# Optimization experiments

Hardware: AMD Instinct MI355X
Metric: run time of the kernel (lower is better)

## Reference

```python
import jax, jax.numpy as jnp
import numpy as np

WH, WW = 7, 7
N_WIN_TOKENS = WH * WW
NUM_HEADS = 8
DIM = 256
HEAD_DIM = DIM // NUM_HEADS
SCALE = HEAD_DIM ** -0.5


def _relative_position_index(wh, ww):
    ch = np.arange(wh)
    cw = np.arange(ww)
    coords = np.stack(np.meshgrid(ch, cw, indexing='ij')).reshape(2, -1)  # [2, N]
    rel = coords[:, :, None] - coords[:, None, :]                         # [2, N, N]
    rel = rel.transpose(1, 2, 0).copy()                                   # [N, N, 2]
    rel[..., 0] += wh - 1
    rel[..., 1] += ww - 1
    rel[..., 0] *= 2 * ww - 1
    return jnp.asarray(rel.sum(-1))                                       # [N, N] int

REL_IDX = _relative_position_index(WH, WW)


def setup_inputs() -> dict:
    key = jax.random.key(0)
    ks = jax.random.split(key, 7)
    B_, nW = 4096, 64
    return {
        'x': jax.random.normal(ks[0], (B_, N_WIN_TOKENS, DIM), jnp.float32),
        'mask': jax.random.normal(ks[1], (nW, N_WIN_TOKENS, N_WIN_TOKENS), jnp.float32),
        'qkv_w': jax.random.normal(ks[2], (3 * DIM, DIM), jnp.float32) * 0.02,
        'qkv_b': jax.random.normal(ks[3], (3 * DIM,), jnp.float32) * 0.02,
        'proj_w': jax.random.normal(ks[4], (DIM, DIM), jnp.float32) * 0.02,
        'proj_b': jax.random.normal(ks[5], (DIM,), jnp.float32) * 0.02,
        'bias_table': jax.random.normal(ks[6], ((2 * WH - 1) * (2 * WW - 1), NUM_HEADS), jnp.float32) * 0.02,
    }


def reference(x, mask, qkv_w, qkv_b, proj_w, proj_b, bias_table):
    B_, N, C = x.shape
    H, D = NUM_HEADS, HEAD_DIM
    qkv = x @ qkv_w.T + qkv_b                           # [B_, N, 3C]
    qkv = qkv.reshape(B_, N, 3, H, D).transpose(2, 0, 3, 1, 4)
    q, k, v = qkv[0], qkv[1], qkv[2]                    # each [B_, H, N, D]
    attn = jnp.einsum('bhnd,bhmd->bhnm', q * SCALE, k)  # [B_, H, N, N]
    bias = bias_table[REL_IDX]                          # [N, N, H]
    attn = attn + bias.transpose(2, 0, 1)[None]
    nW = mask.shape[0]
    attn = attn.reshape(B_ // nW, nW, H, N, N) + mask[None, :, None]
    attn = attn.reshape(B_, H, N, N)
    attn = jax.nn.softmax(attn, axis=-1)
    out = jnp.einsum('bhnm,bhmd->bhnd', attn, v)        # [B_, H, N, D]
    out = out.transpose(0, 2, 1, 3).reshape(B_, N, C)
    out = out @ proj_w.T + proj_b
    return (out, attn)
```

## Files before the change

kernel.cpp:

```cpp
#include <hip/hip_runtime.h>
#include <hip/hip_bf16.h>

typedef __hip_bfloat16 bf16;
typedef __attribute__((ext_vector_type(8))) short bf16x8;
typedef __attribute__((ext_vector_type(4))) float f32x4;

#define NTOK   49
#define CDIM   256
#define NHEADS 8
#define HDIM   32
#define NWIN   64
#define BWIN   4096
#define MROWS  (BWIN * NTOK)
#define QKVC   768
#define SCALE  0.17677669529663687f

__device__ __forceinline__ unsigned short f2bf(float f) {
    unsigned int u = __float_as_uint(f);
    u += 0x7fffu + ((u >> 16) & 1u);
    return (unsigned short)(u >> 16);
}

__device__ __forceinline__ void load_lds16(const void* g, void* l) {
    __builtin_amdgcn_global_load_lds(
        (const __attribute__((address_space(1))) void*)g,
        (__attribute__((address_space(3))) void*)l, 16, 0, 0);
}

__global__ __launch_bounds__(256) void qkv_gemm_mfma(
    const float* __restrict__ X, const float* __restrict__ W,
    const float* __restrict__ bias, bf16* __restrict__ qkv)
{
    __shared__ bf16 As[128 * 64];
    __shared__ bf16 Bs[128 * 64];
    const int tid = threadIdx.x;
    const int wid = tid >> 6;
    const int ln  = tid & 63;

    const int lin   = blockIdx.y * gridDim.x + blockIdx.x;
    const int chunk = (gridDim.x * gridDim.y) >> 3;
    const int swz   = (lin & 7) * chunk + (lin >> 3);
    const int rowBase = (swz / gridDim.x) * 128;
    const int colBase = (swz % gridDim.x) * 128;

    const int wr = wid >> 1, wc = wid & 1;

    f32x4 zero = {0.f, 0.f, 0.f, 0.f};
    f32x4 acc[4][4];
#pragma unroll
    for (int i = 0; i < 4; ++i)
#pragma unroll
        for (int j = 0; j < 4; ++j) acc[i][j] = zero;

    const int srow  = ln >> 3;
    const int gslot = ln & 7;
    const int wslot = gslot ^ srow;
    const size_t aRow0 = (size_t)(rowBase + wid * 32);
    const size_t bRow0 = (size_t)(colBase + wid * 32);

    for (int k0 = 0; k0 < CDIM; k0 += 64) {
        float4 a0[4], a1[4], f0[4], f1[4];
#pragma unroll
        for (int c = 0; c < 4; ++c) {
            const float* gx = X + (aRow0 + c * 8 + srow) * CDIM + k0 + gslot * 8;
            a0[c] = *(const float4*)gx;
            a1[c] = *(const float4*)(gx + 4);
        }
#pragma unroll
        for (int c = 0; c < 4; ++c) {
            const float* gw = W + (size_t)(bRow0 + c * 8 + srow) * CDIM
                              + k0 + gslot * 8;
            f0[c] = *(const float4*)gw;
            f1[c] = *(const float4*)(gw + 4);
        }
#pragma unroll
        for (int c = 0; c < 4; ++c) {
            bf16x8 pk;
            pk[0] = (short)f2bf(a0[c].x); pk[1] = (short)f2bf(a0[c].y);
            pk[2] = (short)f2bf(a0[c].z); pk[3] = (short)f2bf(a0[c].w);
            pk[4] = (short)f2bf(a1[c].x); pk[5] = (short)f2bf(a1[c].y);
            pk[6] = (short)f2bf(a1[c].z); pk[7] = (short)f2bf(a1[c].w);
            *(bf16x8*)((char*)As + (wid * 32 + c * 8 + srow) * 128
                       + (wslot << 4)) = pk;
        }
#pragma unroll
        for (int c = 0; c < 4; ++c) {
            bf16x8 pk;
            pk[0] = (short)f2bf(f0[c].x); pk[1] = (short)f2bf(f0[c].y);
            pk[2] = (short)f2bf(f0[c].z); pk[3] = (short)f2bf(f0[c].w);
            pk[4] = (short)f2bf(f1[c].x); pk[5] = (short)f2bf(f1[c].y);
            pk[6] = (short)f2bf(f1[c].z); pk[7] = (short)f2bf(f1[c].w);
            *(bf16x8*)((char*)Bs + (wid * 32 + c * 8 + srow) * 128
                       + (wslot << 4)) = pk;
        }
        __syncthreads();
#pragma unroll
        for (int kk = 0; kk < 2; ++kk) {
            bf16x8 av[4], bv[4];
#pragma unroll
            for (int m = 0; m < 4; ++m) {
                int r = wr * 64 + m * 16 + (ln & 15);
                int g = kk * 4 + (ln >> 4);
                av[m] = *(const bf16x8*)((const char*)As +
                          (r * 128 + ((g ^ (r & 7)) << 4)));
            }
#pragma unroll
            for (int n = 0; n < 4; ++n) {
                int r = wc * 64 + n * 16 + (ln & 15);
                int g = kk * 4 + (ln >> 4);
                bv[n] = *(const bf16x8*)((const char*)Bs +
                          (r * 128 + ((g ^ (r & 7)) << 4)));
            }
#pragma unroll
            for (int m = 0; m < 4; ++m)
#pragma unroll
                for (int n = 0; n < 4; ++n)
                    acc[m][n] = __builtin_amdgcn_mfma_f32_16x16x32_bf16(
                        av[m], bv[n], acc[m][n], 0, 0, 0);
        }
        __syncthreads();
    }

    const int lq = ln >> 4;
    const int lr = ln & 15;
#pragma unroll
    for (int m = 0; m < 4; ++m) {
#pragma unroll
        for (int q = 0; q < 4; ++q) {
            int row = rowBase + wr * 64 + m * 16 + lq * 4 + q;
            int bw = row / NTOK;
            int nn = row - bw * NTOK;
            bf16* dst0 = qkv + (size_t)bw * 24 * (NTOK * HDIM) + nn * HDIM;
#pragma unroll
            for (int n = 0; n < 4; ++n) {
                int col = colBase + wc * 64 + n * 16 + lr;
                int which = col >> 8, hh = (col >> 5) & 7, dd = col & 31;
                float v = acc[m][n][q] + bias[col];
                dst0[(size_t)(which * 8 + hh) * (NTOK * HDIM) + dd] =
                    __float2bfloat16(v);
            }
        }
    }
}

__global__ __launch_bounds__(256) void attn_mfma_k(
    const bf16* __restrict__ qkv, const float* __restrict__ mask,
    const float* __restrict__ bt, float* __restrict__ attn_out,
    bf16* __restrict__ o_ws)
{
    const int b  = blockIdx.x;
    const int wv = threadIdx.x >> 6;
    const int ln = threadIdx.x & 63;
    const int r  = ln & 15;
    const int g  = ln >> 4;

    __shared__ short vt_all[4][32 * 64];
    __shared__ short ps_all[4][64 * 64];
    __shared__ float mlds[NTOK * NTOK];
    __shared__ float btlds[169 * NHEADS];
    char* vt = (char*)vt_all[wv];
    char* ps = (char*)ps_all[wv];

    const float* mrow = mask + (size_t)(b & (NWIN - 1)) * (NTOK * NTOK);
    for (int e = threadIdx.x; e < NTOK * NTOK; e += 256) mlds[e] = mrow[e];
    for (int e = threadIdx.x; e < 169 * NHEADS; e += 256) btlds[e] = bt[e];
    __syncthreads();

#pragma unroll 1
    for (int hh = 0; hh < 2; ++hh) {
        const int h = wv + hh * 4;
        const bf16* qp = qkv + ((size_t)b * 24 + h)      * (NTOK * HDIM);
        const bf16* kp = qkv + ((size_t)b * 24 + 8 + h)  * (NTOK * HDIM);
        const bf16* vp = qkv + ((size_t)b * 24 + 16 + h) * (NTOK * HDIM);

        bf16x8 qf[4], kf[4];
#pragma unroll
        for (int t = 0; t < 4; ++t) {
            int qi = t * 16 + r; if (qi > 48) qi = 48;
            qf[t] = *(const bf16x8*)(qp + qi * HDIM + g * 8);
            kf[t] = *(const bf16x8*)(kp + qi * HDIM + g * 8);
        }

        bf16x8 vr0 = {0,0,0,0,0,0,0,0}, vr1 = vr0, vr2 = vr0, vr3 = vr0;
        if (ln < NTOK) {
            vr0 = *(const bf16x8*)(vp + ln * HDIM);
            vr1 = *(const bf16x8*)(vp + ln * HDIM + 8);
            vr2 = *(const bf16x8*)(vp + ln * HDIM + 16);
            vr3 = *(const bf16x8*)(vp + ln * HDIM + 24);
        }
#pragma unroll
        for (int d = 0; d < 32; ++d) {
            short val = (d < 8) ? vr0[d & 7] : (d < 16) ? vr1[d & 7]
                      : (d < 24) ? vr2[d & 7] : vr3[d & 7];
            *(short*)(vt + d * 128 + ((((ln >> 3)) ^ (d & 7)) << 4)
                      + (ln & 7) * 2) = val;
        }

        f32x4 zero = {0.f, 0.f, 0.f, 0.f};
        f32x4 s[4][4];
#pragma unroll
        for (int mt = 0; mt < 4; ++mt)
#pragma unroll
            for (int nt = 0; nt < 4; ++nt) s[mt][nt] = zero;
#pragma unroll
        for (int mt = 0; mt < 4; ++mt)
#pragma unroll
            for (int nt = 0; nt < 4; ++nt)
                s[mt][nt] = __builtin_amdgcn_mfma_f32_16x16x32_bf16(
                    kf[mt], qf[nt], s[mt][nt], 0, 0, 0);

        float* aout = attn_out + (((size_t)b * NHEADS + h) * NTOK) * NTOK;
#pragma unroll
        for (int nt = 0; nt < 4; ++nt) {
            const int i = nt * 16 + r;
            const bool iok = (i < NTOK);
            const int ih = (i * 9363) >> 16;
            const int iw = i - ih * 7;
            float sv[4][4];
#pragma unroll
            for (int mt = 0; mt < 4; ++mt)
#pragma unroll
                for (int q = 0; q < 4; ++q) {
                    const int j = mt * 16 + g * 4 + q;
                    float v = -1e30f;
                    if (iok && j < NTOK) {
                        const int jh = (j * 9363) >> 16;
                        const int jw = j - jh * 7;
                        float bias = btlds[((ih - jh + 6) * 13 +
                                            (iw - jw + 6)) * NHEADS + h];
                        v = s[mt][nt][q] * SCALE + bias + mlds[i * NTOK + j];
                    }
                    sv[mt][q] = v;
                }
            float mx = -1e30f;
#pragma unroll
            for (int mt = 0; mt < 4; ++mt)
#pragma unroll
                for (int q = 0; q < 4; ++q) mx = fmaxf(mx, sv[mt][q]);
            mx = fmaxf(mx, __shfl_xor(mx, 16));
            mx = fmaxf(mx, __shfl_xor(mx, 32));
            float sum = 0.f;
#pragma unroll
            for (int mt = 0; mt < 4; ++mt)
#pragma unroll
                for (int q = 0; q < 4; ++q) {
                    sv[mt][q] = __expf(sv[mt][q] - mx);
                    sum += sv[mt][q];
                }
            sum += __shfl_xor(sum, 16);
            sum += __shfl_xor(sum, 32);
            const float inv = 1.0f / sum;
#pragma unroll
            for (int mt = 0; mt < 4; ++mt) {
#pragma unroll
                for (int qh = 0; qh < 2; ++qh) {
                    float p0 = sv[mt][qh * 2]     * inv;
                    float p1 = sv[mt][qh * 2 + 1] * inv;
                    const int j0 = mt * 16 + g * 4 + qh * 2;
                    if (iok) {
                        if (j0 < NTOK)     aout[(size_t)i * NTOK + j0]     = p0;
                        if (j0 + 1 < NTOK) aout[(size_t)i * NTOK + j0 + 1] = p1;
                    }
                    unsigned int pk = (unsigned int)f2bf(p0) |
                                      ((unsigned int)f2bf(p1) << 16);
                    *(unsigned int*)(ps + i * 128 +
                        (((2 * mt + (g >> 1)) ^ (r & 7)) << 4) +
                        (g & 1) * 8 + qh * 4) = pk;
                }
            }
        }

        f32x4 o[4][2];
#pragma unroll
        for (int mt = 0; mt < 4; ++mt)
#pragma unroll
            for (int nt = 0; nt < 2; ++nt) o[mt][nt] = zero;
#pragma unroll
        for (int ks = 0; ks < 2; ++ks) {
            bf16x8 pa[4], vb[2];
#pragma unroll
            for (int mt = 0; mt < 4; ++mt) {
                const int row = mt * 16 + r;
                pa[mt] = *(const bf16x8*)(ps + row * 128 +
                           (((ks * 4 + g) ^ (r & 7)) << 4));
            }
#pragma unroll
            for (int nt = 0; nt < 2; ++nt) {
                const int row = nt * 16 + r;
                vb[nt] = *(const bf16x8*)(vt + row * 128 +
                           (((ks * 4 + g) ^ (r & 7)) << 4));
            }
#pragma unroll
            for (int mt = 0; mt < 4; ++mt)
#pragma unroll
                for (int nt = 0; nt < 2; ++nt)
                    o[mt][nt] = __builtin_amdgcn_mfma_f32_16x16x32_bf16(
                        pa[mt], vb[nt], o[mt][nt], 0, 0, 0);
        }

#pragma unroll
        for (int mt = 0; mt < 4; ++mt) {
#pragma unroll
            for (int q = 0; q < 4; ++q) {
                const int i = mt * 16 + g * 4 + q;
                if (i < NTOK) {
#pragma unroll
                    for (int nt = 0; nt < 2; ++nt) {
                        const int d = nt * 16 + r;
                        o_ws[((size_t)b * NTOK + i) * CDIM + h * HDIM + d] =
                            __float2bfloat16(o[mt][nt][q]);
                    }
                }
            }
        }
    }
}

__global__ __launch_bounds__(256) void proj_gemm_mfma(
    const bf16* __restrict__ A, const float* __restrict__ W,
    const float* __restrict__ bias, float* __restrict__ out)
{
    __shared__ bf16 As[128 * 64];
    __shared__ bf16 Bs[128 * 64];
    const int tid = threadIdx.x;
    const int wid = tid >> 6;
    const int ln  = tid & 63;

    const int lin   = blockIdx.y * gridDim.x + blockIdx.x;
    const int chunk = (gridDim.x * gridDim.y) >> 3;
    const int swz   = (lin & 7) * chunk + (lin >> 3);
    const int rowBase = (swz / gridDim.x) * 128;
    const int colBase = (swz % gridDim.x) * 128;

    const int wr = wid >> 1, wc = wid & 1;

    f32x4 zero = {0.f, 0.f, 0.f, 0.f};
    f32x4 acc[4][4];
#pragma unroll
    for (int i = 0; i < 4; ++i)
#pragma unroll
        for (int j = 0; j < 4; ++j) acc[i][j] = zero;

    const int srow  = ln >> 3;
    const int gslot = ln & 7;
    const int sslotA = gslot ^ srow;
    const int swslotB = gslot ^ srow;
    const size_t aRow0 = (size_t)(rowBase + wid * 32);
    const size_t bRow0 = (size_t)(colBase + wid * 32);

    for (int k0 = 0; k0 < CDIM; k0 += 64) {
#pragma unroll
        for (int c = 0; c < 4; ++c) {
            const bf16* ga = A + (aRow0 + c * 8 + srow) * CDIM + k0 + sslotA * 8;
            load_lds16(ga, &As[(wid * 32 + c * 8) * 64]);
        }
        float4 f0[4], f1[4];
#pragma unroll
        for (int c = 0; c < 4; ++c) {
            const float* gw = W + (size_t)(bRow0 + c * 8 + srow) * CDIM
                              + k0 + gslot * 8;
            f0[c] = *(const float4*)gw;
            f1[c] = *(const float4*)(gw + 4);
        }
#pragma unroll
        for (int c = 0; c < 4; ++c) {
            bf16x8 pk;
            pk[0] = (short)f2bf(f0[c].x); pk[1] = (short)f2bf(f0[c].y);
            pk[2] = (short)f2bf(f0[c].z); pk[3] = (short)f2bf(f0[c].w);
            pk[4] = (short)f2bf(f1[c].x); pk[5] = (short)f2bf(f1[c].y);
            pk[6] = (short)f2bf(f1[c].z); pk[7] = (short)f2bf(f1[c].w);
            *(bf16x8*)((char*)Bs + (wid * 32 + c * 8 + srow) * 128
                       + (swslotB << 4)) = pk;
        }
        __syncthreads();
#pragma unroll
        for (int kk = 0; kk < 2; ++kk) {
            bf16x8 av[4], bv[4];
#pragma unroll
            for (int m = 0; m < 4; ++m) {
                int r = wr * 64 + m * 16 + (ln & 15);
                int g = kk * 4 + (ln >> 4);
                av[m] = *(const bf16x8*)((const char*)As +
                          (r * 128 + ((g ^ (r & 7)) << 4)));
            }
#pragma unroll
            for (int n = 0; n < 4; ++n) {
                int r = wc * 64 + n * 16 + (ln & 15);
                int g = kk * 4 + (ln >> 4);
                bv[n] = *(const bf16x8*)((const char*)Bs +
                          (r * 128 + ((g ^ (r & 7)) << 4)));
            }
#pragma unroll
            for (int m = 0; m < 4; ++m)
#pragma unroll
                for (int n = 0; n < 4; ++n)
                    acc[m][n] = __builtin_amdgcn_mfma_f32_16x16x32_bf16(
                        av[m], bv[n], acc[m][n], 0, 0, 0);
        }
        __syncthreads();
    }

    const int lq = ln >> 4;
    const int lr = ln & 15;
#pragma unroll
    for (int m = 0; m < 4; ++m) {
#pragma unroll
        for (int q = 0; q < 4; ++q) {
            int row = rowBase + wr * 64 + m * 16 + lq * 4 + q;
            float* orow = out + (size_t)row * CDIM;
#pragma unroll
            for (int n = 0; n < 4; ++n) {
                int col = colBase + wc * 64 + n * 16 + lr;
                orow[col] = acc[m][n][q] + bias[col];
            }
        }
    }
}

extern "C" void kernel_launch(void* const* d_in, const int* in_sizes, int n_in,
                              void* d_out, int out_size, void* d_ws, size_t ws_size,
                              hipStream_t stream)
{
    const float* x      = (const float*)d_in[0];
    const float* mask   = (const float*)d_in[1];
    const float* qkv_w  = (const float*)d_in[2];
    const float* qkv_b  = (const float*)d_in[3];
    const float* proj_w = (const float*)d_in[4];
    const float* proj_b = (const float*)d_in[5];
    const float* bt     = (const float*)d_in[6];

    float* out      = (float*)d_out;
    float* attn_out = out + (size_t)MROWS * CDIM;

    bf16* qkv_ws = (bf16*)d_ws;
    bf16* o_ws   = qkv_ws + (size_t)MROWS * QKVC;

    qkv_gemm_mfma<<<dim3(QKVC/128, MROWS/128), 256, 0, stream>>>(
        x, qkv_w, qkv_b, qkv_ws);

    attn_mfma_k<<<dim3(BWIN), 256, 0, stream>>>(qkv_ws, mask, bt,
                                                attn_out, o_ws);

    proj_gemm_mfma<<<dim3(CDIM/128, MROWS/128), 256, 0, stream>>>(
        o_ws, proj_w, proj_b, out);
}
```

Before: 1.129 ms.

## Fuse output projection into attention kernel, pre-converting proj weights to bf16

Removes the separate projection GEMM kernel. Each attention block now stages its per-window head outputs in LDS as a swizzled bf16 tile and multiplies them by a bf16 copy of proj_w, read straight from global/L2. A small pre-kernel converts proj_w to bf16 once per call, replacing the in-loop fp32-to-bf16 conversion. This avoids writing and re-reading the o_ws intermediate through HBM. In exchange, every block re-reads the 128KB weight matrix from cache, and holding both heads' accumulators plus projection accumulators raises register pressure and may lower occupancy.

```diff
diff --git a/kernel.cpp b/kernel.cpp
--- a/kernel.cpp
+++ b/kernel.cpp
@@ -21,10 +21,14 @@
     return (unsigned short)(u >> 16);
 }
 
-__device__ __forceinline__ void load_lds16(const void* g, void* l) {
-    __builtin_amdgcn_global_load_lds(
-        (const __attribute__((address_space(1))) void*)g,
-        (__attribute__((address_space(3))) void*)l, 16, 0, 0);
+__global__ __launch_bounds__(256) void cvt_wp(
+    const float* __restrict__ w, bf16* __restrict__ wb)
+{
+    int i = blockIdx.x * 256 + threadIdx.x;
+    float4 v = ((const float4*)w)[i];
+    ushort4 o;
+    o.x = f2bf(v.x); o.y = f2bf(v.y); o.z = f2bf(v.z); o.w = f2bf(v.w);
+    ((ushort4*)wb)[i] = o;
 }
 
 __global__ __launch_bounds__(256) void qkv_gemm_mfma(
@@ -143,10 +147,11 @@
     }
 }
 
-__global__ __launch_bounds__(256) void attn_mfma_k(
+__global__ __launch_bounds__(256) void attn_proj_k(
     const bf16* __restrict__ qkv, const float* __restrict__ mask,
-    const float* __restrict__ bt, float* __restrict__ attn_out,
-    bf16* __restrict__ o_ws)
+    const float* __restrict__ bt, const bf16* __restrict__ wp,
+    const float* __restrict__ pb, float* __restrict__ attn_out,
+    float* __restrict__ out)
 {
     const int b  = blockIdx.x;
     const int wv = threadIdx.x >> 6;
@@ -154,19 +159,21 @@
     const int r  = ln & 15;
     const int g  = ln >> 4;
 
-    __shared__ short vt_all[4][32 * 64];
-    __shared__ short ps_all[4][64 * 64];
+    __shared__ __align__(16) char smem[49152];
+    char* vt = smem + wv * 4096;
+    char* ps = smem + 16384 + wv * 8192;
     __shared__ float mlds[NTOK * NTOK];
     __shared__ float btlds[169 * NHEADS];
-    char* vt = (char*)vt_all[wv];
-    char* ps = (char*)ps_all[wv];
 
     const float* mrow = mask + (size_t)(b & (NWIN - 1)) * (NTOK * NTOK);
     for (int e = threadIdx.x; e < NTOK * NTOK; e += 256) mlds[e] = mrow[e];
     for (int e = threadIdx.x; e < 169 * NHEADS; e += 256) btlds[e] = bt[e];
     __syncthreads();
 
-#pragma unroll 1
+    f32x4 zero = {0.f, 0.f, 0.f, 0.f};
+    f32x4 oreg[2][4][2];
+
+#pragma unroll
     for (int hh = 0; hh < 2; ++hh) {
         const int h = wv + hh * 4;
         const bf16* qp = qkv + ((size_t)b * 24 + h)      * (NTOK * HDIM);
@@ -196,7 +203,6 @@
                       + (ln & 7) * 2) = val;
         }
 
-        f32x4 zero = {0.f, 0.f, 0.f, 0.f};
         f32x4 s[4][4];
 #pragma unroll
         for (int mt = 0; mt < 4; ++mt)
@@ -270,11 +276,10 @@
             }
         }
 
-        f32x4 o[4][2];
 #pragma unroll
         for (int mt = 0; mt < 4; ++mt)
 #pragma unroll
-            for (int nt = 0; nt < 2; ++nt) o[mt][nt] = zero;
+            for (int nt = 0; nt < 2; ++nt) oreg[hh][mt][nt] = zero;
 #pragma unroll
         for (int ks = 0; ks < 2; ++ks) {
             bf16x8 pa[4], vb[2];
@@ -294,124 +299,73 @@
             for (int mt = 0; mt < 4; ++mt)
 #pragma unroll
                 for (int nt = 0; nt < 2; ++nt)
-                    o[mt][nt] = __builtin_amdgcn_mfma_f32_16x16x32_bf16(
-                        pa[mt], vb[nt], o[mt][nt], 0, 0, 0);
-        }
-
+                    oreg[hh][mt][nt] = __builtin_amdgcn_mfma_f32_16x16x32_bf16(
+                        pa[mt], vb[nt], oreg[hh][mt][nt], 0, 0, 0);
+        }
+    }
+
+    __syncthreads();
+    char* ol = smem;
+#pragma unroll
+    for (int hh = 0; hh < 2; ++hh) {
 #pragma unroll
         for (int mt = 0; mt < 4; ++mt) {
 #pragma unroll
             for (int q = 0; q < 4; ++q) {
-                const int i = mt * 16 + g * 4 + q;
-                if (i < NTOK) {
-#pragma unroll
-                    for (int nt = 0; nt < 2; ++nt) {
-                        const int d = nt * 16 + r;
-                        o_ws[((size_t)b * NTOK + i) * CDIM + h * HDIM + d] =
-                            __float2bfloat16(o[mt][nt][q]);
-                    }
-                }
-            }
-        }
-    }
-}
-
-__global__ __launch_bounds__(256) void proj_gemm_mfma(
-    const bf16* __restrict__ A, const float* __restrict__ W,
-    const float* __restrict__ bias, float* __restrict__ out)
-{
-    __shared__ bf16 As[128 * 64];
-    __shared__ bf16 Bs[128 * 64];
-    const int tid = threadIdx.x;
-    const int wid = tid >> 6;
-    const int ln  = tid & 63;
-
-    const int lin   = blockIdx.y * gridDim.x + blockIdx.x;
-    const int chunk = (gridDim.x * gridDim.y) >> 3;
-    const int swz   = (lin & 7) * chunk + (lin >> 3);
-    const int rowBase = (swz / gridDim.x) * 128;
-    const int colBase = (swz % gridDim.x) * 128;
-
-    const int wr = wid >> 1, wc = wid & 1;
-
-    f32x4 zero = {0.f, 0.f, 0.f, 0.f};
-    f32x4 acc[4][4];
-#pragma unroll
-    for (int i = 0; i < 4; ++i)
-#pragma unroll
-        for (int j = 0; j < 4; ++j) acc[i][j] = zero;
-
-    const int srow  = ln >> 3;
-    const int gslot = ln & 7;
-    const int sslotA = gslot ^ srow;
-    const int swslotB = gslot ^ srow;
-    const size_t aRow0 = (size_t)(rowBase + wid * 32);
-    const size_t bRow0 = (size_t)(colBase + wid * 32);
-
-    for (int k0 = 0; k0 < CDIM; k0 += 64) {
-#pragma unroll
-        for (int c = 0; c < 4; ++c) {
-            const bf16* ga = A + (aRow0 + c * 8 + srow) * CDIM + k0 + sslotA * 8;
-            load_lds16(ga, &As[(wid * 32 + c * 8) * 64]);
-        }
-        float4 f0[4], f1[4];
-#pragma unroll
-        for (int c = 0; c < 4; ++c) {
-            const float* gw = W + (size_t)(bRow0 + c * 8 + srow) * CDIM
-                              + k0 + gslot * 8;
-            f0[c] = *(const float4*)gw;
-            f1[c] = *(const float4*)(gw + 4);
-        }
-#pragma unroll
-        for (int c = 0; c < 4; ++c) {
-            bf16x8 pk;
-            pk[0] = (short)f2bf(f0[c].x); pk[1] = (short)f2bf(f0[c].y);
-            pk[2] = (short)f2bf(f0[c].z); pk[3] = (short)f2bf(f0[c].w);
-            pk[4] = (short)f2bf(f1[c].x); pk[5] = (short)f2bf(f1[c].y);
-            pk[6] = (short)f2bf(f1[c].z); pk[7] = (short)f2bf(f1[c].w);
-            *(bf16x8*)((char*)Bs + (wid * 32 + c * 8 + srow) * 128
-                       + (swslotB << 4)) = pk;
-        }
-        __syncthreads();
-#pragma unroll
-        for (int kk = 0; kk < 2; ++kk) {
-            bf16x8 av[4], bv[4];
-#pragma unroll
-            for (int m = 0; m < 4; ++m) {
-                int r = wr * 64 + m * 16 + (ln & 15);
-                int g = kk * 4 + (ln >> 4);
-                av[m] = *(const bf16x8*)((const char*)As +
-                          (r * 128 + ((g ^ (r & 7)) << 4)));
-            }
-#pragma unroll
-            for (int n = 0; n < 4; ++n) {
-                int r = wc * 64 + n * 16 + (ln & 15);
-                int g = kk * 4 + (ln >> 4);
-                bv[n] = *(const bf16x8*)((const char*)Bs +
-                          (r * 128 + ((g ^ (r & 7)) << 4)));
-            }
-#pragma unroll
-            for (int m = 0; m < 4; ++m)
-#pragma unroll
-                for (int n = 0; n < 4; ++n)
-                    acc[m][n] = __builtin_amdgcn_mfma_f32_16x16x32_bf16(
-                        av[m], bv[n], acc[m][n], 0, 0, 0);
-        }
-        __syncthreads();
-    }
-
-    const int lq = ln >> 4;
-    const int lr = ln & 15;
-#pragma unroll
-    for (int m = 0; m < 4; ++m) {
+                const int row = mt * 16 + g * 4 + q;
+#pragma unroll
+                for (int nt = 0; nt < 2; ++nt) {
+                    const int col = (wv + hh * 4) * HDIM + nt * 16 + r;
+                    *(short*)(ol + row * 512 +
+                              ((((col >> 3)) ^ (row & 7)) << 4) +
+                              (col & 7) * 2) =
+                        (short)f2bf(oreg[hh][mt][nt][q]);
+                }
+            }
+        }
+    }
+    __syncthreads();
+
+    const int wcol = wv * 64;
+    f32x4 pacc[4][4];
+#pragma unroll
+    for (int rt = 0; rt < 4; ++rt)
+#pragma unroll
+        for (int ct = 0; ct < 4; ++ct) pacc[rt][ct] = zero;
+#pragma unroll
+    for (int kf = 0; kf < 8; ++kf) {
+        bf16x8 av[4], bv[4];
+#pragma unroll
+        for (int rt = 0; rt < 4; ++rt) {
+            const int row = rt * 16 + r;
+            av[rt] = *(const bf16x8*)(ol + row * 512 +
+                       (((kf * 4 + g) ^ (row & 7)) << 4));
+        }
+#pragma unroll
+        for (int ct = 0; ct < 4; ++ct) {
+            const int c = wcol + ct * 16 + r;
+            bv[ct] = *(const bf16x8*)(wp + (size_t)c * CDIM + kf * 32 + g * 8);
+        }
+#pragma unroll
+        for (int rt = 0; rt < 4; ++rt)
+#pragma unroll
+            for (int ct = 0; ct < 4; ++ct)
+                pacc[rt][ct] = __builtin_amdgcn_mfma_f32_16x16x32_bf16(
+                    av[rt], bv[ct], pacc[rt][ct], 0, 0, 0);
+    }
+
+    float* ob = out + (size_t)b * NTOK * CDIM;
+#pragma unroll
+    for (int rt = 0; rt < 4; ++rt) {
 #pragma unroll
         for (int q = 0; q < 4; ++q) {
-            int row = rowBase + wr * 64 + m * 16 + lq * 4 + q;
-            float* orow = out + (size_t)row * CDIM;
-#pragma unroll
-            for (int n = 0; n < 4; ++n) {
-                int col = colBase + wc * 64 + n * 16 + lr;
-                orow[col] = acc[m][n][q] + bias[col];
+            const int row = rt * 16 + g * 4 + q;
+            if (row < NTOK) {
+#pragma unroll
+                for (int ct = 0; ct < 4; ++ct) {
+                    const int c = wcol + ct * 16 + r;
+                    ob[(size_t)row * CDIM + c] = pacc[rt][ct][q] + pb[c];
+                }
             }
         }
     }
@@ -433,14 +387,13 @@
     float* attn_out = out + (size_t)MROWS * CDIM;
 
     bf16* qkv_ws = (bf16*)d_ws;
-    bf16* o_ws   = qkv_ws + (size_t)MROWS * QKVC;
+    bf16* wp_b   = qkv_ws + (size_t)MROWS * QKVC;
+
+    cvt_wp<<<64, 256, 0, stream>>>(proj_w, wp_b);
 
     qkv_gemm_mfma<<<dim3(QKVC/128, MROWS/128), 256, 0, stream>>>(
         x, qkv_w, qkv_b, qkv_ws);
 
-    attn_mfma_k<<<dim3(BWIN), 256, 0, stream>>>(qkv_ws, mask, bt,
-                                                attn_out, o_ws);
-
-    proj_gemm_mfma<<<dim3(CDIM/128, MROWS/128), 256, 0, stream>>>(
-        o_ws, proj_w, proj_b, out);
-}
+    attn_proj_k<<<dim3(BWIN), 256, 0, stream>>>(qkv_ws, mask, bt, wp_b,
+                                                proj_b, attn_out, out);
+}
```

Result: no change. 1.130 ms (+0.1%).
